# Kernel optimization log

Measured on AMD Instinct MI355X. Metric: run time of the kernel, lower is better.

Reference implementation:

```python
import jax, jax.numpy as jnp
import numpy as np

B, S, D, H = 2, 4096, 1024, 16
DK = D // H


def setup_inputs() -> dict:
    key = jax.random.key(0)
    ks = jax.random.split(key, 7)
    sc = 1.0 / np.sqrt(D)
    return {
        "q": jax.random.normal(ks[0], (B, S, D), jnp.float32),
        "k": jax.random.normal(ks[1], (B, S, D), jnp.float32),
        "v": jax.random.normal(ks[2], (B, S, D), jnp.float32),
        "wq": jax.random.normal(ks[3], (D, D), jnp.float32) * sc,
        "wk": jax.random.normal(ks[4], (D, D), jnp.float32) * sc,
        "wv": jax.random.normal(ks[5], (D, D), jnp.float32) * sc,
        "w0": jax.random.normal(ks[6], (D, D), jnp.float32) * sc,
    }


def reference(q, k, v, wq, wk, wv, w0):
    # Linear(bias=False): y = x @ W^T  (torch convention, W is [out,in])
    qp = jnp.einsum('bsd,ed->bse', q, wq).reshape(B, S, H, DK).transpose(0, 2, 1, 3)
    kp = jnp.einsum('bsd,ed->bse', k, wk).reshape(B, S, H, DK).transpose(0, 2, 1, 3)
    vp = jnp.einsum('bsd,ed->bse', v, wv).reshape(B, S, H, DK).transpose(0, 2, 1, 3)
    scale = 1.0 / jnp.sqrt(jnp.float32(DK))
    att = jnp.einsum('bhqd,bhkd->bhqk', qp, kp) * scale  # [B,H,S,S]
    att = jax.nn.softmax(att, axis=-1)
    x = jnp.einsum('bhqk,bhkd->bhqd', att, vp)  # [B,H,S,DK]
    x = x.transpose(0, 2, 1, 3).reshape(B, S, D)
    out = jnp.einsum('bsd,ed->bse', x, w0)
    return out
```

## Files before the change

### kernel.cpp

```cpp
#include <hip/hip_runtime.h>
#include <hip/hip_bf16.h>
#include <stdint.h>

#define Bb 2
#define Ss 4096
#define Dd 1024
#define Hh 16
#define DKk 64

typedef __attribute__((ext_vector_type(8))) short bf16x8;
typedef __attribute__((ext_vector_type(4))) float f32x4;
typedef __attribute__((ext_vector_type(16))) float f32x16;

#define MFMA16(a, b, c) __builtin_amdgcn_mfma_f32_32x32x16_bf16(a, b, c, 0, 0, 0)

__device__ __forceinline__ unsigned short f2bf(float f) {
    union { float f; unsigned int u; } x; x.f = f;
    return (unsigned short)((x.u + 0x7fffu + ((x.u >> 16) & 1u)) >> 16);
}

__device__ __forceinline__ void gload16(const void* g, void* l) {
    __builtin_amdgcn_global_load_lds(
        (const __attribute__((address_space(1))) void*)g,
        (__attribute__((address_space(3))) void*)l, 16, 0, 0);
}

__global__ __launch_bounds__(256) void cvt_all(const float* __restrict__ q, const float* __restrict__ k,
                                               const float* __restrict__ v, const float* __restrict__ wq,
                                               const float* __restrict__ wk, const float* __restrict__ wv,
                                               const float* __restrict__ w0, unsigned short* __restrict__ ws) {
    const int QKV4 = 3 * 2097152;
    const int TOT4 = QKV4 + 4 * 262144;
    int i = blockIdx.x * 256 + threadIdx.x;
    const int stride = gridDim.x * 256;
    ushort4* out = (ushort4*)ws;
    for (; i < TOT4; i += stride) {
        const float4* src;
        int di;
        if (i < QKV4) {
            const int r = i >> 21;
            const float* s = r == 0 ? q : (r == 1 ? k : v);
            src = (const float4*)s + (i & 2097151);
            di = i;
        } else {
            const int j = i - QKV4;
            const int r = j >> 18;
            const float* s = r == 0 ? wq : (r == 1 ? wk : (r == 2 ? wv : w0));
            src = (const float4*)s + (j & 262143);
            di = i + 2097152;
        }
        const float4 vv = *src;
        ushort4 o;
        o.x = f2bf(vv.x); o.y = f2bf(vv.y); o.z = f2bf(vv.z); o.w = f2bf(vv.w);
        out[di] = o;
    }
}

template <int MODE>
__global__ __launch_bounds__(256) void gemm_bt(const unsigned short* __restrict__ A,
                                               const unsigned short* __restrict__ W,
                                               void* __restrict__ Y) {
    __shared__ unsigned short As[128 * 32];
    __shared__ unsigned short Bs[128 * 32];
    const int t = threadIdx.x;
    const int wid = t >> 6, lane = t & 63, q4 = lane >> 4, l16 = lane & 15;
    const int wr = wid >> 1, wc = wid & 1;
    const int arow0 = blockIdx.x * 128;
    const int wrow0 = blockIdx.y * 128;
    f32x4 acc[4][4] = {};
    for (int kt = 0; kt < 1024; kt += 32) {
        __syncthreads();
#pragma unroll
        for (int i = 0; i < 2; i++) {
            const int o = i * 4096 + t * 16;
            const int r = o >> 6, c = (o & 63) >> 1;
            gload16(A + (long)(arow0 + r) * 1024 + kt + c, (char*)As + o);
            gload16(W + (long)(wrow0 + r) * 1024 + kt + c, (char*)Bs + o);
        }
        __syncthreads();
        bf16x8 a[4], b[4];
#pragma unroll
        for (int m = 0; m < 4; m++)
            a[m] = *(const bf16x8*)((const char*)As + (wr * 64 + m * 16 + l16) * 64 + q4 * 16);
#pragma unroll
        for (int n = 0; n < 4; n++)
            b[n] = *(const bf16x8*)((const char*)Bs + (wc * 64 + n * 16 + l16) * 64 + q4 * 16);
#pragma unroll
        for (int m = 0; m < 4; m++)
#pragma unroll
            for (int n = 0; n < 4; n++)
                acc[m][n] = __builtin_amdgcn_mfma_f32_16x16x32_bf16(a[m], b[n], acc[m][n], 0, 0, 0);
    }
    const int rb = arow0 + wr * 64, cb = wrow0 + wc * 64;
#pragma unroll
    for (int m = 0; m < 4; m++)
#pragma unroll
        for (int n = 0; n < 4; n++)
#pragma unroll
            for (int r = 0; r < 4; r++) {
                const int row = rb + m * 16 + q4 * 4 + r;
                const int col = cb + n * 16 + l16;
                const float v = acc[m][n][r];
                if (MODE == 0) {
                    ((unsigned short*)Y)[(long)row * 1024 + col] = f2bf(v);
                } else if (MODE == 1) {
                    const int bb = row >> 12, s = row & 4095;
                    const int hh = col >> 6, dk = col & 63;
                    ((unsigned short*)Y)[(((long)(bb * Hh + hh) * DKk + dk) << 12) + s] = f2bf(v);
                } else if (MODE == 3) {
                    ((unsigned short*)Y)[(long)row * 1024 + col] = f2bf(v * 0.1803368801111244f);
                } else {
                    ((float*)Y)[(long)row * 1024 + col] = v;
                }
            }
}

__global__ __launch_bounds__(256, 2) void attn_fwd(const unsigned short* __restrict__ qp,
                                                   const unsigned short* __restrict__ kp,
                                                   const unsigned short* __restrict__ vt,
                                                   unsigned short* __restrict__ xo) {
    __shared__ __align__(16) char smem[32768];
    const int t = threadIdx.x;
    const int wid = t >> 6, lane = t & 63;
    const int l5 = lane & 31;
    const int ihi = lane >> 5;
    const int swz5 = (l5 & 7) ^ ((l5 >> 3) & 3);
    const int qt = blockIdx.x, h = blockIdx.y, b = blockIdx.z;
    const unsigned short* qbase = qp + ((long)b * Ss + qt * 256) * Dd + h * 64;
    const unsigned short* kbase = kp + (long)b * Ss * Dd + h * 64;
    const unsigned short* vbase = vt + (long)(b * Hh + h) * DKk * Ss;

    const int r0 = t >> 3;
    const int s0 = t & 7;
    const int cb0 = s0 ^ (r0 & 7) ^ ((r0 >> 3) & 3);
    const int o0 = t * 16;
    const unsigned short* qsrc = qbase + (long)r0 * Dd + cb0 * 8;
    const unsigned short* ksrc = kbase + (long)r0 * Dd + cb0 * 8;
    const unsigned short* vsrc = vbase + (long)r0 * Ss + cb0 * 8;

#pragma unroll
    for (int i = 0; i < 8; i++)
        gload16(qsrc + (long)i * 32 * Dd, smem + i * 4096 + o0);
    asm volatile("s_waitcnt vmcnt(0)" ::: "memory");
    __builtin_amdgcn_s_barrier();
    asm volatile("" ::: "memory");

    bf16x8 bQ[2][4];
#pragma unroll
    for (int qb = 0; qb < 2; qb++)
#pragma unroll
        for (int m = 0; m < 4; m++) {
            const int chunk = wid * 2 + qb;
            const int slot = (m * 2 + ihi) ^ swz5;
            bQ[qb][m] = *(const bf16x8*)(smem + chunk * 4096 + l5 * 128 + (slot << 4));
        }
    asm volatile("s_waitcnt lgkmcnt(0)" ::: "memory");
    __builtin_amdgcn_s_barrier();
    asm volatile("" ::: "memory");

    gload16(ksrc,                  smem + o0);
    gload16(ksrc + 32 * Dd,        smem + 4096 + o0);
    gload16(vsrc,                  smem + 8192 + o0);
    gload16(vsrc + 32 * Ss,        smem + 12288 + o0);
    gload16(ksrc + 64 * Dd,        smem + 16384 + o0);
    gload16(ksrc + 96 * Dd,        smem + 20480 + o0);
    gload16(vsrc + 64,             smem + 24576 + o0);
    gload16(vsrc + 32 * Ss + 64,   smem + 28672 + o0);
    const unsigned short* pk = ksrc + 128 * Dd;
    const unsigned short* pv = vsrc + 128;
    asm volatile("s_waitcnt vmcnt(4)" ::: "memory");
    __builtin_amdgcn_s_barrier();
    asm volatile("" ::: "memory");

    int adm[4];
#pragma unroll
    for (int m = 0; m < 4; m++)
        adm[m] = l5 * 128 + ((((m * 2 + ihi) ^ swz5)) << 4);

    f32x16 accO[2][2] = {};
    float li[2] = {0.f, 0.f};

    for (int kt2 = 0; kt2 < 64; kt2 += 2) {
#pragma unroll
        for (int hf = 0; hf < 2; hf++) {
            const int kt = kt2 + hf;
            const int BO = hf << 14;
            const char* Kc = smem + BO;
            const char* Vc = smem + BO + 8192;
            f32x16 accS[2][2] = {};
            __builtin_amdgcn_s_setprio(1);
#pragma unroll
            for (int m = 0; m < 4; m++) {
                const bf16x8 aK0 = *(const bf16x8*)(Kc + adm[m]);
                const bf16x8 aK1 = *(const bf16x8*)(Kc + 4096 + adm[m]);
                accS[0][0] = MFMA16(aK0, bQ[0][m], accS[0][0]);
                accS[0][1] = MFMA16(aK1, bQ[0][m], accS[0][1]);
                accS[1][0] = MFMA16(aK0, bQ[1][m], accS[1][0]);
                accS[1][1] = MFMA16(aK1, bQ[1][m], accS[1][1]);
            }
            float ps0 = 0.f, ps1 = 0.f;
#pragma unroll
            for (int m = 0; m < 4; m++) {
                const bf16x8 aV0 = *(const bf16x8*)(Vc + adm[m]);
                const bf16x8 aV1 = *(const bf16x8*)(Vc + 4096 + adm[m]);
                const int kb = m >> 1, sx = (m & 1) * 2;
#pragma unroll
                for (int qb = 0; qb < 2; qb++) {
                    unsigned w00, w01, w10, w11;
                    float gs;
                    {
                        const float a0 = __builtin_amdgcn_exp2f(accS[qb][kb][4 * sx + 0]);
                        const float a1 = __builtin_amdgcn_exp2f(accS[qb][kb][4 * sx + 1]);
                        const float a2 = __builtin_amdgcn_exp2f(accS[qb][kb][4 * sx + 2]);
                        const float a3 = __builtin_amdgcn_exp2f(accS[qb][kb][4 * sx + 3]);
                        const float b0 = __builtin_amdgcn_exp2f(accS[qb][kb][4 * sx + 4]);
                        const float b1 = __builtin_amdgcn_exp2f(accS[qb][kb][4 * sx + 5]);
                        const float b2 = __builtin_amdgcn_exp2f(accS[qb][kb][4 * sx + 6]);
                        const float b3 = __builtin_amdgcn_exp2f(accS[qb][kb][4 * sx + 7]);
                        gs = ((a0 + a1) + (a2 + a3)) + ((b0 + b1) + (b2 + b3));
                        asm("v_cvt_pk_bf16_f32 %0, %1, %2" : "=v"(w00) : "v"(a0), "v"(a1));
                        asm("v_cvt_pk_bf16_f32 %0, %1, %2" : "=v"(w01) : "v"(a2), "v"(a3));
                        asm("v_cvt_pk_bf16_f32 %0, %1, %2" : "=v"(w10) : "v"(b0), "v"(b1));
                        asm("v_cvt_pk_bf16_f32 %0, %1, %2" : "=v"(w11) : "v"(b2), "v"(b3));
                    }
                    if (qb == 0) ps0 += gs; else ps1 += gs;
                    asm("v_permlane32_swap_b32 %0, %1" : "+v"(w00), "+v"(w10));
                    asm("v_permlane32_swap_b32 %0, %1" : "+v"(w01), "+v"(w11));
                    union { unsigned u[4]; bf16x8 v; } fr;
                    fr.u[0] = w00; fr.u[1] = w01; fr.u[2] = w10; fr.u[3] = w11;
                    accO[0][qb] = MFMA16(aV0, fr.v, accO[0][qb]);
                    accO[1][qb] = MFMA16(aV1, fr.v, accO[1][qb]);
                }
            }
            __builtin_amdgcn_s_setprio(0);
            li[0] += ps0 + __shfl_xor(ps0, 32, 64);
            li[1] += ps1 + __shfl_xor(ps1, 32, 64);
            __builtin_amdgcn_s_barrier();
            asm volatile("" ::: "memory");
            if (kt < 62) {
                char* dst = smem + BO;
                gload16(pk,            dst + o0);
                gload16(pk + 32 * Dd,  dst + 4096 + o0);
                gload16(pv,            dst + 8192 + o0);
                gload16(pv + 32 * Ss,  dst + 12288 + o0);
                pk += 64 * Dd;
                pv += 64;
                asm volatile("s_waitcnt vmcnt(4)" ::: "memory");
            } else {
                asm volatile("s_waitcnt vmcnt(0)" ::: "memory");
            }
            __builtin_amdgcn_s_barrier();
            asm volatile("" ::: "memory");
        }
    }

#pragma unroll
    for (int qb = 0; qb < 2; qb++) {
        const float rli = 1.0f / li[qb];
        const int chunk = wid * 2 + qb;
#pragma unroll
        for (int dblk = 0; dblk < 2; dblk++)
#pragma unroll
            for (int tt = 0; tt < 8; tt++) {
                const unsigned short b0 = f2bf(accO[dblk][qb][2 * tt] * rli);
                const unsigned short b1 = f2bf(accO[dblk][qb][2 * tt + 1] * rli);
                const int slot = (dblk * 4 + (tt >> 1)) ^ swz5;
                const int phys = chunk * 4096 + l5 * 128 + (slot << 4) + ihi * 8 + (tt & 1) * 4;
                *(unsigned*)(smem + phys) = ((unsigned)b1 << 16) | b0;
            }
    }
    __syncthreads();
#pragma unroll
    for (int p = 0; p < 8; p++) {
        const uint4 val = *(const uint4*)(smem + p * 4096 + o0);
        const long row = (long)qt * 256 + p * 32 + r0;
        *(uint4*)(xo + ((long)b * Ss + row) * Dd + h * 64 + cb0 * 8) = val;
    }
}

extern "C" void kernel_launch(void* const* d_in, const int* in_sizes, int n_in,
                              void* d_out, int out_size, void* d_ws, size_t ws_size,
                              hipStream_t stream) {
    const float* q  = (const float*)d_in[0];
    const float* k  = (const float*)d_in[1];
    const float* v  = (const float*)d_in[2];
    const float* wq = (const float*)d_in[3];
    const float* wk = (const float*)d_in[4];
    const float* wv = (const float*)d_in[5];
    const float* w0 = (const float*)d_in[6];

    unsigned short* ws = (unsigned short*)d_ws;
    const long NE = (long)Bb * Ss * Dd;
    unsigned short* qb  = ws;
    unsigned short* kb  = ws + NE;
    unsigned short* vb  = ws + 2 * NE;
    unsigned short* x1  = ws + 3 * NE;
    unsigned short* wqb = ws + 4 * NE;
    unsigned short* wkb = wqb + 1048576;
    unsigned short* wvb = wkb + 1048576;
    unsigned short* w0b = wvb + 1048576;

    cvt_all<<<2048, 256, 0, stream>>>(q, k, v, wq, wk, wv, w0, ws);

    dim3 gg(64, 8);
    gemm_bt<3><<<gg, 256, 0, stream>>>(qb, wqb, x1);
    gemm_bt<0><<<gg, 256, 0, stream>>>(kb, wkb, qb);
    gemm_bt<1><<<gg, 256, 0, stream>>>(vb, wvb, kb);
    dim3 ga(16, 16, 2);
    attn_fwd<<<ga, 256, 0, stream>>>(x1, qb, kb, vb);
    gemm_bt<2><<<gg, 256, 0, stream>>>(vb, w0b, (float*)d_out);
}
```

Measured before the change: 264.3 us.

## Split attention query tile across 8 waves instead of 4

The attention kernel now launches 512 threads per block, so each of 8 waves owns 32 query rows instead of 64. Per-wave register state (Q fragments, S and O accumulators) halves, and launch bounds target 4 blocks per CU. Each K/V tile in LDS is now shared by twice as many waves, and each thread issues half as many global-to-LDS loads. In exchange, each wave does less MFMA work between barriers, so barrier overhead per unit of work rises.

```diff
diff --git a/kernel.cpp b/kernel.cpp
--- a/kernel.cpp
+++ b/kernel.cpp
@@ -115,7 +115,7 @@
             }
 }
 
-__global__ __launch_bounds__(256, 2) void attn_fwd(const unsigned short* __restrict__ qp,
+__global__ __launch_bounds__(512, 4) void attn_fwd(const unsigned short* __restrict__ qp,
                                                    const unsigned short* __restrict__ kp,
                                                    const unsigned short* __restrict__ vt,
                                                    unsigned short* __restrict__ xo) {
@@ -131,44 +131,37 @@
     const unsigned short* vbase = vt + (long)(b * Hh + h) * DKk * Ss;
 
     const int r0 = t >> 3;
-    const int s0 = t & 7;
-    const int cb0 = s0 ^ (r0 & 7) ^ ((r0 >> 3) & 3);
+    const int s0i = t & 7;
+    const int cb0 = s0i ^ (r0 & 7) ^ ((r0 >> 3) & 3);
     const int o0 = t * 16;
     const unsigned short* qsrc = qbase + (long)r0 * Dd + cb0 * 8;
     const unsigned short* ksrc = kbase + (long)r0 * Dd + cb0 * 8;
     const unsigned short* vsrc = vbase + (long)r0 * Ss + cb0 * 8;
 
 #pragma unroll
-    for (int i = 0; i < 8; i++)
-        gload16(qsrc + (long)i * 32 * Dd, smem + i * 4096 + o0);
+    for (int i = 0; i < 4; i++)
+        gload16(qsrc + (long)i * 64 * Dd, smem + i * 8192 + o0);
     asm volatile("s_waitcnt vmcnt(0)" ::: "memory");
     __builtin_amdgcn_s_barrier();
     asm volatile("" ::: "memory");
 
-    bf16x8 bQ[2][4];
-#pragma unroll
-    for (int qb = 0; qb < 2; qb++)
-#pragma unroll
-        for (int m = 0; m < 4; m++) {
-            const int chunk = wid * 2 + qb;
-            const int slot = (m * 2 + ihi) ^ swz5;
-            bQ[qb][m] = *(const bf16x8*)(smem + chunk * 4096 + l5 * 128 + (slot << 4));
-        }
+    bf16x8 bQ[4];
+#pragma unroll
+    for (int m = 0; m < 4; m++) {
+        const int slot = (m * 2 + ihi) ^ swz5;
+        bQ[m] = *(const bf16x8*)(smem + wid * 4096 + l5 * 128 + (slot << 4));
+    }
     asm volatile("s_waitcnt lgkmcnt(0)" ::: "memory");
     __builtin_amdgcn_s_barrier();
     asm volatile("" ::: "memory");
 
-    gload16(ksrc,                  smem + o0);
-    gload16(ksrc + 32 * Dd,        smem + 4096 + o0);
-    gload16(vsrc,                  smem + 8192 + o0);
-    gload16(vsrc + 32 * Ss,        smem + 12288 + o0);
-    gload16(ksrc + 64 * Dd,        smem + 16384 + o0);
-    gload16(ksrc + 96 * Dd,        smem + 20480 + o0);
-    gload16(vsrc + 64,             smem + 24576 + o0);
-    gload16(vsrc + 32 * Ss + 64,   smem + 28672 + o0);
+    gload16(ksrc,                smem + o0);
+    gload16(vsrc,                smem + 8192 + o0);
+    gload16(ksrc + 64 * Dd,      smem + 16384 + o0);
+    gload16(vsrc + 64,           smem + 24576 + o0);
     const unsigned short* pk = ksrc + 128 * Dd;
     const unsigned short* pv = vsrc + 128;
-    asm volatile("s_waitcnt vmcnt(4)" ::: "memory");
+    asm volatile("s_waitcnt vmcnt(2)" ::: "memory");
     __builtin_amdgcn_s_barrier();
     asm volatile("" ::: "memory");
 
@@ -177,8 +170,8 @@
     for (int m = 0; m < 4; m++)
         adm[m] = l5 * 128 + ((((m * 2 + ihi) ^ swz5)) << 4);
 
-    f32x16 accO[2][2] = {};
-    float li[2] = {0.f, 0.f};
+    f32x16 accO[2] = {};
+    float li = 0.f;
 
     for (int kt2 = 0; kt2 < 64; kt2 += 2) {
 #pragma unroll
@@ -187,65 +180,55 @@
             const int BO = hf << 14;
             const char* Kc = smem + BO;
             const char* Vc = smem + BO + 8192;
-            f32x16 accS[2][2] = {};
+            f32x16 accS[2] = {};
             __builtin_amdgcn_s_setprio(1);
 #pragma unroll
             for (int m = 0; m < 4; m++) {
                 const bf16x8 aK0 = *(const bf16x8*)(Kc + adm[m]);
                 const bf16x8 aK1 = *(const bf16x8*)(Kc + 4096 + adm[m]);
-                accS[0][0] = MFMA16(aK0, bQ[0][m], accS[0][0]);
-                accS[0][1] = MFMA16(aK1, bQ[0][m], accS[0][1]);
-                accS[1][0] = MFMA16(aK0, bQ[1][m], accS[1][0]);
-                accS[1][1] = MFMA16(aK1, bQ[1][m], accS[1][1]);
-            }
-            float ps0 = 0.f, ps1 = 0.f;
+                accS[0] = MFMA16(aK0, bQ[m], accS[0]);
+                accS[1] = MFMA16(aK1, bQ[m], accS[1]);
+            }
+            float ps = 0.f;
 #pragma unroll
             for (int m = 0; m < 4; m++) {
                 const bf16x8 aV0 = *(const bf16x8*)(Vc + adm[m]);
                 const bf16x8 aV1 = *(const bf16x8*)(Vc + 4096 + adm[m]);
                 const int kb = m >> 1, sx = (m & 1) * 2;
-#pragma unroll
-                for (int qb = 0; qb < 2; qb++) {
-                    unsigned w00, w01, w10, w11;
-                    float gs;
-                    {
-                        const float a0 = __builtin_amdgcn_exp2f(accS[qb][kb][4 * sx + 0]);
-                        const float a1 = __builtin_amdgcn_exp2f(accS[qb][kb][4 * sx + 1]);
-                        const float a2 = __builtin_amdgcn_exp2f(accS[qb][kb][4 * sx + 2]);
-                        const float a3 = __builtin_amdgcn_exp2f(accS[qb][kb][4 * sx + 3]);
-                        const float b0 = __builtin_amdgcn_exp2f(accS[qb][kb][4 * sx + 4]);
-                        const float b1 = __builtin_amdgcn_exp2f(accS[qb][kb][4 * sx + 5]);
-                        const float b2 = __builtin_amdgcn_exp2f(accS[qb][kb][4 * sx + 6]);
-                        const float b3 = __builtin_amdgcn_exp2f(accS[qb][kb][4 * sx + 7]);
-                        gs = ((a0 + a1) + (a2 + a3)) + ((b0 + b1) + (b2 + b3));
-                        asm("v_cvt_pk_bf16_f32 %0, %1, %2" : "=v"(w00) : "v"(a0), "v"(a1));
-                        asm("v_cvt_pk_bf16_f32 %0, %1, %2" : "=v"(w01) : "v"(a2), "v"(a3));
-                        asm("v_cvt_pk_bf16_f32 %0, %1, %2" : "=v"(w10) : "v"(b0), "v"(b1));
-                        asm("v_cvt_pk_bf16_f32 %0, %1, %2" : "=v"(w11) : "v"(b2), "v"(b3));
-                    }
-                    if (qb == 0) ps0 += gs; else ps1 += gs;
-                    asm("v_permlane32_swap_b32 %0, %1" : "+v"(w00), "+v"(w10));
-                    asm("v_permlane32_swap_b32 %0, %1" : "+v"(w01), "+v"(w11));
-                    union { unsigned u[4]; bf16x8 v; } fr;
-                    fr.u[0] = w00; fr.u[1] = w01; fr.u[2] = w10; fr.u[3] = w11;
-                    accO[0][qb] = MFMA16(aV0, fr.v, accO[0][qb]);
-                    accO[1][qb] = MFMA16(aV1, fr.v, accO[1][qb]);
+                unsigned w00, w01, w10, w11;
+                {
+                    const float a0 = __builtin_amdgcn_exp2f(accS[kb][4 * sx + 0]);
+                    const float a1 = __builtin_amdgcn_exp2f(accS[kb][4 * sx + 1]);
+                    const float a2 = __builtin_amdgcn_exp2f(accS[kb][4 * sx + 2]);
+                    const float a3 = __builtin_amdgcn_exp2f(accS[kb][4 * sx + 3]);
+                    const float b0 = __builtin_amdgcn_exp2f(accS[kb][4 * sx + 4]);
+                    const float b1 = __builtin_amdgcn_exp2f(accS[kb][4 * sx + 5]);
+                    const float b2 = __builtin_amdgcn_exp2f(accS[kb][4 * sx + 6]);
+                    const float b3 = __builtin_amdgcn_exp2f(accS[kb][4 * sx + 7]);
+                    ps += ((a0 + a1) + (a2 + a3)) + ((b0 + b1) + (b2 + b3));
+                    asm("v_cvt_pk_bf16_f32 %0, %1, %2" : "=v"(w00) : "v"(a0), "v"(a1));
+                    asm("v_cvt_pk_bf16_f32 %0, %1, %2" : "=v"(w01) : "v"(a2), "v"(a3));
+                    asm("v_cvt_pk_bf16_f32 %0, %1, %2" : "=v"(w10) : "v"(b0), "v"(b1));
+                    asm("v_cvt_pk_bf16_f32 %0, %1, %2" : "=v"(w11) : "v"(b2), "v"(b3));
                 }
+                asm("v_permlane32_swap_b32 %0, %1" : "+v"(w00), "+v"(w10));
+                asm("v_permlane32_swap_b32 %0, %1" : "+v"(w01), "+v"(w11));
+                union { unsigned u[4]; bf16x8 v; } fr;
+                fr.u[0] = w00; fr.u[1] = w01; fr.u[2] = w10; fr.u[3] = w11;
+                accO[0] = MFMA16(aV0, fr.v, accO[0]);
+                accO[1] = MFMA16(aV1, fr.v, accO[1]);
             }
             __builtin_amdgcn_s_setprio(0);
-            li[0] += ps0 + __shfl_xor(ps0, 32, 64);
-            li[1] += ps1 + __shfl_xor(ps1, 32, 64);
+            li += ps + __shfl_xor(ps, 32, 64);
             __builtin_amdgcn_s_barrier();
             asm volatile("" ::: "memory");
             if (kt < 62) {
                 char* dst = smem + BO;
-                gload16(pk,            dst + o0);
-                gload16(pk + 32 * Dd,  dst + 4096 + o0);
-                gload16(pv,            dst + 8192 + o0);
-                gload16(pv + 32 * Ss,  dst + 12288 + o0);
+                gload16(pk, dst + o0);
+                gload16(pv, dst + 8192 + o0);
                 pk += 64 * Dd;
                 pv += 64;
-                asm volatile("s_waitcnt vmcnt(4)" ::: "memory");
+                asm volatile("s_waitcnt vmcnt(2)" ::: "memory");
             } else {
                 asm volatile("s_waitcnt vmcnt(0)" ::: "memory");
             }
@@ -254,26 +237,22 @@
         }
     }
 
-#pragma unroll
-    for (int qb = 0; qb < 2; qb++) {
-        const float rli = 1.0f / li[qb];
-        const int chunk = wid * 2 + qb;
-#pragma unroll
-        for (int dblk = 0; dblk < 2; dblk++)
-#pragma unroll
-            for (int tt = 0; tt < 8; tt++) {
-                const unsigned short b0 = f2bf(accO[dblk][qb][2 * tt] * rli);
-                const unsigned short b1 = f2bf(accO[dblk][qb][2 * tt + 1] * rli);
-                const int slot = (dblk * 4 + (tt >> 1)) ^ swz5;
-                const int phys = chunk * 4096 + l5 * 128 + (slot << 4) + ihi * 8 + (tt & 1) * 4;
-                *(unsigned*)(smem + phys) = ((unsigned)b1 << 16) | b0;
-            }
-    }
+    const float rli = 1.0f / li;
+#pragma unroll
+    for (int dblk = 0; dblk < 2; dblk++)
+#pragma unroll
+        for (int tt = 0; tt < 8; tt++) {
+            const unsigned short b0 = f2bf(accO[dblk][2 * tt] * rli);
+            const unsigned short b1 = f2bf(accO[dblk][2 * tt + 1] * rli);
+            const int slot = (dblk * 4 + (tt >> 1)) ^ swz5;
+            const int phys = wid * 4096 + l5 * 128 + (slot << 4) + ihi * 8 + (tt & 1) * 4;
+            *(unsigned*)(smem + phys) = ((unsigned)b1 << 16) | b0;
+        }
     __syncthreads();
 #pragma unroll
-    for (int p = 0; p < 8; p++) {
-        const uint4 val = *(const uint4*)(smem + p * 4096 + o0);
-        const long row = (long)qt * 256 + p * 32 + r0;
+    for (int p = 0; p < 4; p++) {
+        const uint4 val = *(const uint4*)(smem + p * 8192 + o0);
+        const long row = (long)qt * 256 + p * 64 + r0;
         *(uint4*)(xo + ((long)b * Ss + row) * Dd + h * 64 + cb0 * 8) = val;
     }
 }
@@ -307,6 +286,6 @@
     gemm_bt<0><<<gg, 256, 0, stream>>>(kb, wkb, qb);
     gemm_bt<1><<<gg, 256, 0, stream>>>(vb, wvb, kb);
     dim3 ga(16, 16, 2);
-    attn_fwd<<<ga, 256, 0, stream>>>(x1, qb, kb, vb);
+    attn_fwd<<<ga, 512, 0, stream>>>(x1, qb, kb, vb);
     gemm_bt<2><<<gg, 256, 0, stream>>>(vb, w0b, (float*)d_out);
 }
```

After: 268.1 us (median of 2 runs). Within noise of the previous version (+1.4%).
